# Kernel tuning notes

Measured on AMD Instinct MI355X. Metric: run time of the kernel, lower is better.

## Reference

```python
import jax, jax.numpy as jnp
import numpy as np

D_MODEL = 64
D_STATE = 16
D_CONV = 4
EXPAND = 2
D_INNER = EXPAND * D_MODEL        # 128
DT_RANK = max(1, D_MODEL // 16)   # 4 (mamba_ssm default ceil(d_model/16))
BATCH, HH, WW = 2, 128, 128


def setup_inputs() -> dict:
    key = jax.random.key(0)
    ks = jax.random.split(key, 10)
    def norm(k, shape, sc=0.05):
        return jax.random.normal(k, shape, jnp.float32) * sc
    # A initialized as in mamba_ssm: A = 1..d_state per channel, stored as log
    A_log = jnp.log(jnp.tile(jnp.arange(1, D_STATE + 1, dtype=jnp.float32), (4, D_INNER, 1)))
    return {
        "x": jax.random.normal(ks[0], (BATCH, D_MODEL, HH, WW), jnp.float32),
        "in_w": norm(ks[1], (4, 2 * D_INNER, D_MODEL)),
        "conv_w": norm(ks[2], (4, D_INNER, D_CONV), 0.2),
        "conv_b": jnp.zeros((4, D_INNER), jnp.float32),
        "xp_w": norm(ks[3], (4, DT_RANK + 2 * D_STATE, D_INNER)),
        "dtp_w": norm(ks[4], (4, D_INNER, DT_RANK), 0.2),
        "dtp_b": jnp.full((4, D_INNER), -4.0, jnp.float32) + norm(ks[5], (4, D_INNER), 0.5),
        "A_log": A_log,
        "Dp": jnp.ones((4, D_INNER), jnp.float32),
        "out_w": norm(ks[6], (4, D_MODEL, D_INNER)),
        "fuse_w": norm(ks[7], (D_MODEL, 4 * D_MODEL)),
        "fuse_b": jnp.zeros((D_MODEL,), jnp.float32),
        "ln_g": jnp.ones((D_MODEL,), jnp.float32),
        "ln_b": jnp.zeros((D_MODEL,), jnp.float32),
    }


def _mamba(xseq, in_w, conv_w, conv_b, xp_w, dtp_w, dtp_b, A_log, Dp, out_w):
    # xseq: (N, L, d_model) -> (N, L, d_model). Single-direction Mamba block.
    N, L, _ = xseq.shape
    xz = xseq @ in_w.T                       # (N, L, 2*d_inner)
    u, z = jnp.split(xz, 2, axis=-1)
    # causal depthwise conv1d, kernel width D_CONV
    up = jnp.pad(u, ((0, 0), (D_CONV - 1, 0), (0, 0)))
    uc = conv_b + sum(up[:, k:k + L, :] * conv_w[:, k][None, None, :] for k in range(D_CONV))
    uc = jax.nn.silu(uc)
    dbl = uc @ xp_w.T                        # (N, L, dt_rank + 2*d_state)
    dt = jax.nn.softplus(dbl[..., :DT_RANK] @ dtp_w.T + dtp_b)   # (N, L, d_inner)
    Bm = dbl[..., DT_RANK:DT_RANK + D_STATE]                     # (N, L, d_state)
    Cm = dbl[..., DT_RANK + D_STATE:]                            # (N, L, d_state)
    A = -jnp.exp(A_log)                                          # (d_inner, d_state)

    def step(h, inp):
        dt_t, B_t, C_t, u_t = inp            # (N,d_inner),(N,d_state),(N,d_state),(N,d_inner)
        h = h * jnp.exp(dt_t[..., None] * A) + (dt_t * u_t)[..., None] * B_t[:, None, :]
        y = jnp.einsum('nds,ns->nd', h, C_t)
        return h, y

    h0 = jnp.zeros((N, D_INNER, D_STATE), xseq.dtype)
    _, ys = jax.lax.scan(step, h0, (dt.swapaxes(0, 1), Bm.swapaxes(0, 1),
                                    Cm.swapaxes(0, 1), uc.swapaxes(0, 1)))
    y = ys.swapaxes(0, 1) + uc * Dp
    y = y * jax.nn.silu(z)
    return y @ out_w.T


def reference(x, in_w, conv_w, conv_b, xp_w, dtp_w, dtp_b, A_log, Dp, out_w,
              fuse_w, fuse_b, ln_g, ln_b):
    B, C, H, W = x.shape
    xhwc = x.transpose(0, 2, 3, 1)           # (B,H,W,C)
    xwhc = x.transpose(0, 3, 2, 1)           # (B,W,H,C)
    d0 = xhwc.reshape(B * H, W, C)                         # horizontal fwd
    d1 = xhwc[:, :, ::-1, :].reshape(B * H, W, C)          # horizontal bwd
    d2 = xwhc.reshape(B * W, H, C)                         # vertical fwd
    d3 = xwhc[:, :, ::-1, :].reshape(B * W, H, C)          # vertical bwd
    xd = jnp.stack([d0, d1, d2, d3])         # (4, B*S, S, C) since H == W
    ys = jax.vmap(_mamba)(xd, in_w, conv_w, conv_b, xp_w, dtp_w, dtp_b, A_log, Dp, out_w)
    y0 = ys[0].reshape(B, H, W, C)
    y1 = ys[1].reshape(B, H, W, C)[:, :, ::-1, :]
    y2 = ys[2].reshape(B, W, H, C).transpose(0, 2, 1, 3)
    y3 = ys[3].reshape(B, W, H, C)[:, :, ::-1, :].transpose(0, 2, 1, 3)
    cat = jnp.concatenate([y0, y1, y2, y3], axis=-1)       # (B,H,W,4C)
    f = cat @ fuse_w.T + fuse_b                            # 1x1 conv
    mu = f.mean(-1, keepdims=True)
    var = f.var(-1, keepdims=True)
    f = (f - mu) * jax.lax.rsqrt(var + 1e-5) * ln_g + ln_b # LayerNorm over C
    f = jax.nn.silu(f)
    return f.transpose(0, 3, 1, 2)                          # (B,C,H,W)
```

## Files before the change

### kernel.cpp

```cpp
#include <hip/hip_runtime.h>
#include <math.h>


typedef __attribute__((ext_vector_type(8))) short short8;
typedef __attribute__((ext_vector_type(4))) float f32x4;

__device__ __forceinline__ unsigned short f2bf(float f) {
  unsigned int u = __float_as_uint(f);
  u += 0x7fffu + ((u >> 16) & 1u);
  return (unsigned short)(u >> 16);
}
__device__ __forceinline__ float bf2f(unsigned short h) {
  return __uint_as_float(((unsigned int)h) << 16);
}
__device__ __forceinline__ float siluf(float x) { return x / (1.f + __expf(-x)); }

__global__ void k0_prep(const float* __restrict__ out_w, const float* __restrict__ fuse_w,
                        const float* __restrict__ in_w, const float* __restrict__ xp_w,
                        const float* __restrict__ x,
                        unsigned short* __restrict__ MT16, unsigned short* __restrict__ W16,
                        unsigned short* __restrict__ XW16, unsigned short* __restrict__ XH) {
  __shared__ unsigned short sT[64*132];
  int blk = blockIdx.x;
  int tid = threadIdx.x;
  if (blk < 128) {
    int idx = blk * 256 + tid;
    int d   = idx & 127;
    int o   = (idx >> 7) & 63;
    int dir = idx >> 13;
    float acc = 0.f;
    #pragma unroll 8
    for (int j = 0; j < 64; ++j)
      acc += out_w[(dir*64 + j)*128 + d] * fuse_w[o*256 + dir*64 + j];
    MT16[o*512 + dir*128 + d] = f2bf(acc);
  } else if (blk < 160) {
    int t = (blk - 128) * 256 + tid;
    int base = t * 8;
    float4 v0 = *(const float4*)(in_w + base);
    float4 v1 = *(const float4*)(in_w + base + 4);
    uint4 pk;
    pk.x = (unsigned int)f2bf(v0.x) | ((unsigned int)f2bf(v0.y) << 16);
    pk.y = (unsigned int)f2bf(v0.z) | ((unsigned int)f2bf(v0.w) << 16);
    pk.z = (unsigned int)f2bf(v1.x) | ((unsigned int)f2bf(v1.y) << 16);
    pk.w = (unsigned int)f2bf(v1.z) | ((unsigned int)f2bf(v1.w) << 16);
    *(uint4*)(W16 + base) = pk;
  } else if (blk < 164) {
    int t = (blk - 160) * 256 + tid;
    for (int pid = t; pid < 4*48*128; pid += 1024) {
      int dir = pid / 6144;
      int rem = pid - dir*6144;
      int row = rem >> 7, c = rem & 127;
      XW16[pid] = (row < 36) ? f2bf(xp_w[dir*4608 + row*128 + c]) : (unsigned short)0;
    }
  } else {
    int idx = blk - 164;
    int b = idx >> 7, h = idx & 127;
    for (int f = tid*4; f < 8192; f += 1024) {
      int c = f >> 7, w = f & 127;
      float4 v = *(const float4*)(x + (((size_t)(b*64 + c)*128 + h)*128 + w));
      sT[c*132 + w + 0] = f2bf(v.x);
      sT[c*132 + w + 1] = f2bf(v.y);
      sT[c*132 + w + 2] = f2bf(v.z);
      sT[c*132 + w + 3] = f2bf(v.w);
    }
    __syncthreads();
    for (int f = tid*8; f < 8192; f += 2048) {
      int w = f >> 6, c0 = f & 63;
      unsigned int pk[4];
      #pragma unroll
      for (int p = 0; p < 4; ++p) {
        unsigned int lo = sT[(c0 + p*2 + 0)*132 + w];
        unsigned int hi = sT[(c0 + p*2 + 1)*132 + w];
        pk[p] = lo | (hi << 16);
      }
      uint4 v; v.x = pk[0]; v.y = pk[1]; v.z = pk[2]; v.w = pk[3];
      *(uint4*)(XH + (((size_t)(b*128 + h)*128 + w)*64 + c0)) = v;
    }
  }
}

__global__ void kT2(const unsigned short* __restrict__ XH, unsigned short* __restrict__ XW) {
  int idx = blockIdx.x;
  int b = idx >> 7, h = idx & 127;
  int tid = threadIdx.x;
  const unsigned short* src = XH + ((size_t)(b*128 + h)*128)*64;
  for (int f = tid*8; f < 8192; f += 2048) {
    int w = f >> 6, c = f & 63;
    uint4 v = *(const uint4*)(src + f);
    *(uint4*)(XW + (((size_t)(b*128 + w)*128 + h)*64 + c)) = v;
  }
}

__global__ __launch_bounds__(256, 3) void k1_front(
    const unsigned short* __restrict__ XH, const unsigned short* __restrict__ XW,
    const unsigned short* __restrict__ W16, const unsigned short* __restrict__ XW16,
    const float* __restrict__ conv_w, const float* __restrict__ conv_b,
    const float* __restrict__ dtp_w, const float* __restrict__ dtp_b,
    const float* __restrict__ A_log, const float* __restrict__ Dp,
    unsigned short* __restrict__ YF)
{
  __shared__ __align__(16) char smem[53248];
  float* sBCf         = (float*)smem;
  unsigned short* sUC = (unsigned short*)(smem + 18432);

  const int tid = threadIdx.x;
  const int dir = blockIdx.x >> 8;
  const int n   = blockIdx.x & 255;
  const int b   = n >> 7;
  const int r   = n & 127;
  const int n_all = dir*256 + n;

  const unsigned short* xsrc = (dir < 2 ? XH : XW) + ((size_t)(b*128 + r)*128)*64;

  const int wave = tid >> 6;
  const int lane = tid & 63;
  const int m16 = lane & 15;
  const int quad = lane >> 4;
  const int tb0 = wave * 32;
  const int st0 = tb0 + m16;
  const int st1 = tb0 + 16 + m16;
  const int sp0 = (dir & 1) ? (127 - st0) : st0;
  const int sp1 = (dir & 1) ? (127 - st1) : st1;

  unsigned int zpk[2][8][2];

  {
    short8 bfr[2][2];
    #pragma unroll
    for (int ks = 0; ks < 2; ++ks) {
      bfr[0][ks] = *(const short8*)(xsrc + sp0*64 + ks*32 + quad*8);
      bfr[1][ks] = *(const short8*)(xsrc + sp1*64 + ks*32 + quad*8);
    }
    const unsigned short* Wd = W16 + (size_t)dir * 16384;

    for (int rt = 0; rt < 8; ++rt) {
      short8 af[2];
      #pragma unroll
      for (int ks = 0; ks < 2; ++ks)
        af[ks] = *(const short8*)(Wd + (rt*16 + m16)*64 + ks*32 + quad*8);
      #pragma unroll
      for (int tt = 0; tt < 2; ++tt) {
        f32x4 acc = {0.f, 0.f, 0.f, 0.f};
        acc = __builtin_amdgcn_mfma_f32_16x16x32_bf16(af[0], bfr[tt][0], acc, 0, 0, 0);
        acc = __builtin_amdgcn_mfma_f32_16x16x32_bf16(af[1], bfr[tt][1], acc, 0, 0, 0);
        const int tok = tt ? st1 : st0;
        const int r0 = rt*16 + quad*4;
        uint2 u2;
        u2.x = (unsigned int)f2bf(acc[0]) | ((unsigned int)f2bf(acc[1]) << 16);
        u2.y = (unsigned int)f2bf(acc[2]) | ((unsigned int)f2bf(acc[3]) << 16);
        *(uint2*)(sUC + tok*136 + r0) = u2;
      }
    }
    #pragma unroll
    for (int k = 0; k < 8; ++k) {
      short8 af[2];
      #pragma unroll
      for (int ks = 0; ks < 2; ++ks)
        af[ks] = *(const short8*)(Wd + ((8+k)*16 + m16)*64 + ks*32 + quad*8);
      #pragma unroll
      for (int tt = 0; tt < 2; ++tt) {
        f32x4 acc = {0.f, 0.f, 0.f, 0.f};
        acc = __builtin_amdgcn_mfma_f32_16x16x32_bf16(af[0], bfr[tt][0], acc, 0, 0, 0);
        acc = __builtin_amdgcn_mfma_f32_16x16x32_bf16(af[1], bfr[tt][1], acc, 0, 0, 0);
        zpk[tt][k][0] = (unsigned int)f2bf(siluf(acc[0])) | ((unsigned int)f2bf(siluf(acc[1])) << 16);
        zpk[tt][k][1] = (unsigned int)f2bf(siluf(acc[2])) | ((unsigned int)f2bf(siluf(acc[3])) << 16);
      }
    }
  }
  __syncthreads();

  {
    const int d = tid & 127;
    const int half = tid >> 7;
    const int lc0 = half * 64;
    const float* cw = conv_w + (size_t)(dir*128 + d)*4;
    const float c0w = cw[0], c1w = cw[1], c2w = cw[2], c3w = cw[3];
    const float cb = conv_b[dir*128 + d];
    float p0 = half ? bf2f(sUC[(lc0-3)*136 + d]) : 0.f;
    float p1 = half ? bf2f(sUC[(lc0-2)*136 + d]) : 0.f;
    float p2 = half ? bf2f(sUC[(lc0-1)*136 + d]) : 0.f;
    __syncthreads();
    for (int l = lc0; l < lc0 + 64; ++l) {
      float cur = bf2f(sUC[l*136 + d]);
      float v = cb + c0w*p0 + c1w*p1 + c2w*p2 + c3w*cur;
      sUC[l*136 + d] = f2bf(siluf(v));
      p0 = p1; p1 = p2; p2 = cur;
    }
  }
  __syncthreads();

  {
    short8 bfr[2][4];
    #pragma unroll
    for (int tt = 0; tt < 2; ++tt)
      #pragma unroll
      for (int ks = 0; ks < 4; ++ks)
        bfr[tt][ks] = *(const short8*)(sUC + (tt ? st1 : st0)*136 + ks*32 + quad*8);

    const unsigned short* XWd = XW16 + (size_t)dir * (48*128);

    for (int rt = 0; rt < 3; ++rt) {
      short8 af[4];
      #pragma unroll
      for (int ks = 0; ks < 4; ++ks)
        af[ks] = *(const short8*)(XWd + (rt*16 + m16)*128 + ks*32 + quad*8);
      #pragma unroll
      for (int tt = 0; tt < 2; ++tt) {
        f32x4 acc = {0.f, 0.f, 0.f, 0.f};
        #pragma unroll
        for (int ks = 0; ks < 4; ++ks)
          acc = __builtin_amdgcn_mfma_f32_16x16x32_bf16(af[ks], bfr[tt][ks], acc, 0, 0, 0);
        const int tok = tt ? st1 : st0;
        const int r0 = rt*16 + quad*4;
        if (r0 == 0) {
          float4 v; v.x = acc[0]; v.y = acc[1]; v.z = acc[2]; v.w = acc[3];
          *(float4*)(smem + 18432 + tok*272 + 256) = v;
        } else if (r0 < 36) {
          float4 v; v.x = acc[0]; v.y = acc[1]; v.z = acc[2]; v.w = acc[3];
          *(float4*)(sBCf + tok*36 + (r0 - 4)) = v;
        }
      }
    }
  }
  __syncthreads();

  {
    const int d = tid >> 1;
    const int p = tid & 1;
    const float* dwp = dtp_w + (size_t)(dir*128 + d) * 4;
    const float dw0 = dwp[0], dw1 = dwp[1], dw2 = dwp[2], dw3 = dwp[3];
    const float db = dtp_b[dir*128 + d];
    const float dpv = Dp[dir*128 + d];

    float Av[8];
    bool fast = true;
    #pragma unroll
    for (int j = 0; j < 8; ++j) {
      float a = -__expf(A_log[((size_t)(dir*128 + d))*16 + p*8 + j]);
      Av[j] = a;
      if (fabsf((-a) - (float)(p*8 + j + 1)) > 1e-3f) fast = false;
    }

    float h[8];
    #pragma unroll
    for (int j = 0; j < 8; ++j) h[j] = 0.f;

    #define SCAN_LOAD                                                     \
      float4 q0 = *(const float4*)(smem + 18432 + l*272 + 256);           \
      float4 b0 = *(const float4*)(sBCf + l*36 + p*8);                    \
      float4 b1 = *(const float4*)(sBCf + l*36 + p*8 + 4);                \
      float4 c0 = *(const float4*)(sBCf + l*36 + 16 + p*8);               \
      float4 c1 = *(const float4*)(sBCf + l*36 + 16 + p*8 + 4);           \
      float Bv[8] = {b0.x,b0.y,b0.z,b0.w, b1.x,b1.y,b1.z,b1.w};           \
      float Cv[8] = {c0.x,c0.y,c0.z,c0.w, c1.x,c1.y,c1.z,c1.w};           \
      float dr = q0.x*dw0 + q0.y*dw1 + q0.z*dw2 + q0.w*dw3 + db;          \
      float dt = (dr > 20.f) ? dr : __logf(1.f + __expf(dr));             \
      float u = bf2f(sUC[l*136 + d]);                                     \
      float dtu = dt * u;

    if (fast) {
      for (int l = 0; l < 128; ++l) {
        SCAN_LOAD
        float E = __expf(-dt);
        float E2 = E*E, E4 = E2*E2, E8 = E4*E4;
        float e = p ? E8 : 1.f;
        float yp = 0.f;
        #pragma unroll
        for (int j = 0; j < 8; ++j) {
          e *= E;
          h[j] = h[j]*e + dtu*Bv[j];
          yp += h[j]*Cv[j];
        }
        float ysum = yp + __shfl_xor(yp, 1, 64);
        if (p == 0) sUC[l*136 + d] = f2bf(ysum + u*dpv);
      }
    } else {
      for (int l = 0; l < 128; ++l) {
        SCAN_LOAD
        float yp = 0.f;
        #pragma unroll
        for (int j = 0; j < 8; ++j) {
          float ej = __expf(dt*Av[j]);
          h[j] = h[j]*ej + dtu*Bv[j];
          yp += h[j]*Cv[j];
        }
        float ysum = yp + __shfl_xor(yp, 1, 64);
        if (p == 0) sUC[l*136 + d] = f2bf(ysum + u*dpv);
      }
    }
    #undef SCAN_LOAD
  }
  __syncthreads();

  #pragma unroll
  for (int tt = 0; tt < 2; ++tt) {
    const int st = tt ? st1 : st0;
    size_t rowbase;
    if (dir < 2)       rowbase = ((size_t)n_all*128 + st)*128;
    else if (dir == 2) rowbase = ((size_t)(512 + b*128 + st)*128 + r)*128;
    else               rowbase = ((size_t)(768 + b*128 + (127-st))*128 + r)*128;
    #pragma unroll
    for (int k = 0; k < 8; ++k) {
      const int dz = 16*k + quad*4;
      uint2 yv = *(const uint2*)(sUC + st*136 + dz);
      float y0 = __uint_as_float(yv.x << 16);
      float y1 = __uint_as_float(yv.x & 0xffff0000u);
      float y2 = __uint_as_float(yv.y << 16);
      float y3 = __uint_as_float(yv.y & 0xffff0000u);
      unsigned int z01 = zpk[tt][k][0], z23 = zpk[tt][k][1];
      float z0 = __uint_as_float(z01 << 16);
      float z1 = __uint_as_float(z01 & 0xffff0000u);
      float z2 = __uint_as_float(z23 << 16);
      float z3 = __uint_as_float(z23 & 0xffff0000u);
      uint2 ov;
      ov.x = (unsigned int)f2bf(y0*z0) | ((unsigned int)f2bf(y1*z1) << 16);
      ov.y = (unsigned int)f2bf(y2*z2) | ((unsigned int)f2bf(y3*z3) << 16);
      *(uint2*)(YF + rowbase + dz) = ov;
    }
  }
}

__global__ __launch_bounds__(256, 2) void k3_fuse(
    const unsigned short* __restrict__ YF, const unsigned short* __restrict__ MT16,
    const float* __restrict__ fuse_b, const float* __restrict__ ln_g,
    const float* __restrict__ ln_b, float* __restrict__ out)
{
  __shared__ __align__(16) unsigned short sYB[64*520];

  const int tid = threadIdx.x;
  const int blk = blockIdx.x;
  const int b = blk >> 8;
  const int rr2 = blk & 255;
  const int h = rr2 >> 1;
  const int w0 = (rr2 & 1) * 64;

  for (int f = tid*8; f < 32768; f += 2048) {
    int dirg = f >> 13;
    int rem = f & 8191;
    int tok = rem >> 7;
    int dd = rem & 127;
    int X = (dirg == 1) ? (127 - w0 - tok) : (w0 + tok);
    size_t base = ((size_t)(dirg*256 + b*128 + h)*128 + X)*128 + dd;
    *(uint4*)(sYB + tok*520 + dirg*128 + dd) = *(const uint4*)(YF + base);
  }
  __syncthreads();

  const int wave = tid >> 6;
  const int lane = tid & 63;
  const int m16 = lane & 15;
  const int quad = lane >> 4;
  const int tok = wave*16 + m16;

  short8 bfr[16];
  #pragma unroll
  for (int jt = 0; jt < 16; ++jt)
    bfr[jt] = *(const short8*)(sYB + tok*520 + jt*32 + quad*8);

  float facc[4][4];
  #pragma unroll
  for (int mt = 0; mt < 4; ++mt) {
    f32x4 acc = {0.f, 0.f, 0.f, 0.f};
    #pragma unroll
    for (int jt = 0; jt < 16; ++jt) {
      short8 af = *(const short8*)(MT16 + (size_t)(mt*16 + m16)*512 + jt*32 + quad*8);
      acc = __builtin_amdgcn_mfma_f32_16x16x32_bf16(af, bfr[jt], acc, 0, 0, 0);
    }
    facc[mt][0] = acc[0]; facc[mt][1] = acc[1]; facc[mt][2] = acc[2]; facc[mt][3] = acc[3];
  }

  float fv[16];
  float s1 = 0.f, s2 = 0.f;
  #pragma unroll
  for (int mt = 0; mt < 4; ++mt)
    #pragma unroll
    for (int rr = 0; rr < 4; ++rr) {
      int o = mt*16 + quad*4 + rr;
      float v = facc[mt][rr] + fuse_b[o];
      fv[mt*4 + rr] = v;
      s1 += v; s2 += v*v;
    }
  s1 += __shfl_xor(s1, 16, 64); s1 += __shfl_xor(s1, 32, 64);
  s2 += __shfl_xor(s2, 16, 64); s2 += __shfl_xor(s2, 32, 64);
  float mu = s1 * (1.f/64.f);
  float var = s2 * (1.f/64.f) - mu*mu;
  float rs = rsqrtf(var + 1e-5f);

  #pragma unroll
  for (int mt = 0; mt < 4; ++mt)
    #pragma unroll
    for (int rr = 0; rr < 4; ++rr) {
      int o = mt*16 + quad*4 + rr;
      float v = (fv[mt*4 + rr] - mu) * rs * ln_g[o] + ln_b[o];
      out[((size_t)(b*64 + o)*128 + h)*128 + (w0 + tok)] = siluf(v);
    }
}

extern "C" void kernel_launch(void* const* d_in, const int* in_sizes, int n_in,
                              void* d_out, int out_size, void* d_ws, size_t ws_size,
                              hipStream_t stream) {
  const float* x      = (const float*)d_in[0];
  const float* in_w   = (const float*)d_in[1];
  const float* conv_w = (const float*)d_in[2];
  const float* conv_b = (const float*)d_in[3];
  const float* xp_w   = (const float*)d_in[4];
  const float* dtp_w  = (const float*)d_in[5];
  const float* dtp_b  = (const float*)d_in[6];
  const float* A_log  = (const float*)d_in[7];
  const float* Dp     = (const float*)d_in[8];
  const float* out_w  = (const float*)d_in[9];
  const float* fuse_w = (const float*)d_in[10];
  const float* fuse_b = (const float*)d_in[11];
  const float* ln_g   = (const float*)d_in[12];
  const float* ln_b   = (const float*)d_in[13];
  float* out = (float*)d_out;

  char* ws = (char*)d_ws;
  unsigned short* YF   = (unsigned short*)(ws);
  unsigned short* MT16 = (unsigned short*)(ws + 33554432);
  unsigned short* W16  = (unsigned short*)(ws + 33619968);
  unsigned short* XW16 = (unsigned short*)(ws + 33751040);
  unsigned short* XH   = (unsigned short*)(ws + 33800192);
  unsigned short* XWt  = (unsigned short*)(ws + 37994496);

  k0_prep<<<dim3(420), dim3(256), 0, stream>>>(out_w, fuse_w, in_w, xp_w, x,
                                               MT16, W16, XW16, XH);
  kT2<<<dim3(256), dim3(256), 0, stream>>>(XH, XWt);
  k1_front<<<dim3(1024), dim3(256), 0, stream>>>(XH, XWt, W16, XW16, conv_w, conv_b,
                                                 dtp_w, dtp_b, A_log, Dp, YF);
  k3_fuse<<<dim3(512), dim3(256), 0, stream>>>(YF, MT16, fuse_b, ln_g, ln_b, out);
}
```

Baseline: 229.4 us.

## Use packed bf16 conversion, fast rcp silu, interleaved conv chains, exp reuse in scan

Replaces manual bf16 rounding with the HIP bf16 intrinsics, including a packed two-value conversion that may map to a hardware pack instruction on gfx950. SiLU now uses a fast reciprocal instead of a division. The depthwise conv loop interleaves two independent 32-step chains per thread to expose more instruction-level parallelism. In the scan, exp(-softplus(dr)) is computed as 1/(1+exp(dr)), reusing the exponential already computed for softplus, which drops one exp per step; this differs slightly from the original when dr > 20, where softplus falls back to dr.

```diff
diff --git a/kernel.cpp b/kernel.cpp
--- a/kernel.cpp
+++ b/kernel.cpp
@@ -1,19 +1,28 @@
 #include <hip/hip_runtime.h>
+#include <hip/hip_bf16.h>
 #include <math.h>
 
 
 typedef __attribute__((ext_vector_type(8))) short short8;
 typedef __attribute__((ext_vector_type(4))) float f32x4;
 
+__device__ __forceinline__ unsigned int pk2bf(float a, float b) {
+  __hip_bfloat162 h = __float22bfloat162_rn(make_float2(a, b));
+  unsigned int u;
+  __builtin_memcpy(&u, &h, 4);
+  return u;
+}
 __device__ __forceinline__ unsigned short f2bf(float f) {
-  unsigned int u = __float_as_uint(f);
-  u += 0x7fffu + ((u >> 16) & 1u);
-  return (unsigned short)(u >> 16);
+  __hip_bfloat16 h = __float2bfloat16(f);
+  unsigned short s;
+  __builtin_memcpy(&s, &h, 2);
+  return s;
 }
 __device__ __forceinline__ float bf2f(unsigned short h) {
   return __uint_as_float(((unsigned int)h) << 16);
 }
-__device__ __forceinline__ float siluf(float x) { return x / (1.f + __expf(-x)); }
+__device__ __forceinline__ float fastrcp(float x) { return __builtin_amdgcn_rcpf(x); }
+__device__ __forceinline__ float siluf(float x) { return x * fastrcp(1.f + __expf(-x)); }
 
 __global__ void k0_prep(const float* __restrict__ out_w, const float* __restrict__ fuse_w,
                         const float* __restrict__ in_w, const float* __restrict__ xp_w,
@@ -39,10 +48,10 @@
     float4 v0 = *(const float4*)(in_w + base);
     float4 v1 = *(const float4*)(in_w + base + 4);
     uint4 pk;
-    pk.x = (unsigned int)f2bf(v0.x) | ((unsigned int)f2bf(v0.y) << 16);
-    pk.y = (unsigned int)f2bf(v0.z) | ((unsigned int)f2bf(v0.w) << 16);
-    pk.z = (unsigned int)f2bf(v1.x) | ((unsigned int)f2bf(v1.y) << 16);
-    pk.w = (unsigned int)f2bf(v1.z) | ((unsigned int)f2bf(v1.w) << 16);
+    pk.x = pk2bf(v0.x, v0.y);
+    pk.y = pk2bf(v0.z, v0.w);
+    pk.z = pk2bf(v1.x, v1.y);
+    pk.w = pk2bf(v1.z, v1.w);
     *(uint4*)(W16 + base) = pk;
   } else if (blk < 164) {
     int t = (blk - 160) * 256 + tid;
@@ -146,8 +155,8 @@
         const int tok = tt ? st1 : st0;
         const int r0 = rt*16 + quad*4;
         uint2 u2;
-        u2.x = (unsigned int)f2bf(acc[0]) | ((unsigned int)f2bf(acc[1]) << 16);
-        u2.y = (unsigned int)f2bf(acc[2]) | ((unsigned int)f2bf(acc[3]) << 16);
+        u2.x = pk2bf(acc[0], acc[1]);
+        u2.y = pk2bf(acc[2], acc[3]);
         *(uint2*)(sUC + tok*136 + r0) = u2;
       }
     }
@@ -162,8 +171,8 @@
         f32x4 acc = {0.f, 0.f, 0.f, 0.f};
         acc = __builtin_amdgcn_mfma_f32_16x16x32_bf16(af[0], bfr[tt][0], acc, 0, 0, 0);
         acc = __builtin_amdgcn_mfma_f32_16x16x32_bf16(af[1], bfr[tt][1], acc, 0, 0, 0);
-        zpk[tt][k][0] = (unsigned int)f2bf(siluf(acc[0])) | ((unsigned int)f2bf(siluf(acc[1])) << 16);
-        zpk[tt][k][1] = (unsigned int)f2bf(siluf(acc[2])) | ((unsigned int)f2bf(siluf(acc[3])) << 16);
+        zpk[tt][k][0] = pk2bf(siluf(acc[0]), siluf(acc[1]));
+        zpk[tt][k][1] = pk2bf(siluf(acc[2]), siluf(acc[3]));
       }
     }
   }
@@ -172,19 +181,27 @@
   {
     const int d = tid & 127;
     const int half = tid >> 7;
-    const int lc0 = half * 64;
+    const int ca = half * 32;
+    const int cb2 = (half + 2) * 32;
     const float* cw = conv_w + (size_t)(dir*128 + d)*4;
     const float c0w = cw[0], c1w = cw[1], c2w = cw[2], c3w = cw[3];
-    const float cb = conv_b[dir*128 + d];
-    float p0 = half ? bf2f(sUC[(lc0-3)*136 + d]) : 0.f;
-    float p1 = half ? bf2f(sUC[(lc0-2)*136 + d]) : 0.f;
-    float p2 = half ? bf2f(sUC[(lc0-1)*136 + d]) : 0.f;
+    const float cbv = conv_b[dir*128 + d];
+    float a0 = half ? bf2f(sUC[(ca-3)*136 + d]) : 0.f;
+    float a1 = half ? bf2f(sUC[(ca-2)*136 + d]) : 0.f;
+    float a2 = half ? bf2f(sUC[(ca-1)*136 + d]) : 0.f;
+    float b0 = bf2f(sUC[(cb2-3)*136 + d]);
+    float b1 = bf2f(sUC[(cb2-2)*136 + d]);
+    float b2 = bf2f(sUC[(cb2-1)*136 + d]);
     __syncthreads();
-    for (int l = lc0; l < lc0 + 64; ++l) {
-      float cur = bf2f(sUC[l*136 + d]);
-      float v = cb + c0w*p0 + c1w*p1 + c2w*p2 + c3w*cur;
-      sUC[l*136 + d] = f2bf(siluf(v));
-      p0 = p1; p1 = p2; p2 = cur;
+    for (int i = 0; i < 32; ++i) {
+      float curA = bf2f(sUC[(ca+i)*136 + d]);
+      float curB = bf2f(sUC[(cb2+i)*136 + d]);
+      float vA = cbv + c0w*a0 + c1w*a1 + c2w*a2 + c3w*curA;
+      float vB = cbv + c0w*b0 + c1w*b1 + c2w*b2 + c3w*curB;
+      sUC[(ca+i)*136 + d]  = f2bf(siluf(vA));
+      sUC[(cb2+i)*136 + d] = f2bf(siluf(vB));
+      a0 = a1; a1 = a2; a2 = curA;
+      b0 = b1; b1 = b2; b2 = curB;
     }
   }
   __syncthreads();
@@ -254,14 +271,15 @@
       float Bv[8] = {b0.x,b0.y,b0.z,b0.w, b1.x,b1.y,b1.z,b1.w};           \
       float Cv[8] = {c0.x,c0.y,c0.z,c0.w, c1.x,c1.y,c1.z,c1.w};           \
       float dr = q0.x*dw0 + q0.y*dw1 + q0.z*dw2 + q0.w*dw3 + db;          \
-      float dt = (dr > 20.f) ? dr : __logf(1.f + __expf(dr));             \
+      float te = __expf(dr);                                              \
+      float dt = (dr > 20.f) ? dr : __logf(1.f + te);                     \
       float u = bf2f(sUC[l*136 + d]);                                     \
       float dtu = dt * u;
 
     if (fast) {
       for (int l = 0; l < 128; ++l) {
         SCAN_LOAD
-        float E = __expf(-dt);
+        float E = fastrcp(1.f + te);
         float E2 = E*E, E4 = E2*E2, E8 = E4*E4;
         float e = p ? E8 : 1.f;
         float yp = 0.f;
@@ -313,8 +331,8 @@
       float z2 = __uint_as_float(z23 << 16);
       float z3 = __uint_as_float(z23 & 0xffff0000u);
       uint2 ov;
-      ov.x = (unsigned int)f2bf(y0*z0) | ((unsigned int)f2bf(y1*z1) << 16);
-      ov.y = (unsigned int)f2bf(y2*z2) | ((unsigned int)f2bf(y3*z3) << 16);
+      ov.x = pk2bf(y0*z0, y1*z1);
+      ov.y = pk2bf(y2*z2, y3*z3);
       *(uint2*)(YF + rowbase + dz) = ov;
     }
   }
```

Result: faster. 213.6 us (-6.8%).
